# Kernel tuning notes

Measured on AMD Instinct MI355X. Metric: run time of the kernel, lower is better.

## Reference

```python
import jax, jax.numpy as jnp
import numpy as np

N = 50000      # nodes
E = 800000     # edges (avg degree 16)
F_IN = 128     # mod2_dim
DIMS = [(F_IN, 64), (64, 128), (128, 256), (256, 256)]
OUT_DIM = 1    # final_prediction: Linear(256, 1)


def setup_inputs() -> dict:
    key = jax.random.key(0)
    ks = jax.random.split(key, 16)
    inp = {
        "x": jax.random.normal(ks[0], (N, F_IN), jnp.float32),
        "edge_index": jax.random.randint(ks[1], (2, E), 0, N, dtype=jnp.int64),
        "edge_attr": jax.random.uniform(ks[2], (E,), jnp.float32),
    }
    for i, (fin, fout) in enumerate(DIMS):
        inp[f"W{i+1}"] = jax.random.normal(ks[3 + i], (fin, fout), jnp.float32) / np.sqrt(fin)
        inp[f"b{i+1}"] = jnp.zeros((fout,), jnp.float32)
    inp["Wf"] = jax.random.normal(ks[8], (256, OUT_DIM), jnp.float32) / np.sqrt(256.0)
    inp["bf"] = jnp.zeros((OUT_DIM,), jnp.float32)
    return inp


def _gcn_conv(x, src, dst, w, W, b):
    """PyG GCNConv: D^-1/2 (A + I) D^-1/2 X W + b with edge weights.
    src/dst/w already include self-loops (weight 1)."""
    h = x @ W                                            # [N, Fout]
    deg = jax.ops.segment_sum(w, dst, num_segments=N)    # weighted in-degree
    dinv = jnp.where(deg > 0, jax.lax.rsqrt(deg), 0.0)
    norm = dinv[src] * w * dinv[dst]                     # [E+N]
    msg = h[src] * norm[:, None]                         # gather + scale
    out = jax.ops.segment_sum(msg, dst, num_segments=N)  # scatter-add
    return out + b


def reference(x, edge_index, edge_attr, W1, b1, W2, b2, W3, b3, W4, b4, Wf, bf):
    loops = jnp.arange(N, dtype=edge_index.dtype)
    src = jnp.concatenate([edge_index[0], loops])
    dst = jnp.concatenate([edge_index[1], loops])
    w = jnp.concatenate([edge_attr, jnp.ones((N,), edge_attr.dtype)])

    h = x
    for W, b in ((W1, b1), (W2, b2), (W3, b3), (W4, b4)):
        h = jax.nn.relu(_gcn_conv(h, src, dst, w, W, b))
        # F.dropout with training=False -> identity (eval mode)
    out = h @ Wf + bf
    return out
```

## Files before the change

kernel.cpp:

```cpp
#include <hip/hip_runtime.h>
#include <math.h>


typedef _Float16 half8 __attribute__((ext_vector_type(8)));
typedef _Float16 half4_t __attribute__((ext_vector_type(4)));
typedef float f32x4 __attribute__((ext_vector_type(4)));

#define SCAN_CHUNK 2048
#define DEG_SCALE 67108864.0f
#define DEG_MASK ((1ULL << 42) - 1)

__global__ __launch_bounds__(256) void k_init(unsigned long long* __restrict__ packed,
                                              int n) {
    int i = blockIdx.x * 256 + threadIdx.x;
    if (i < n) packed[i] = (1ULL << 26);
}

__global__ __launch_bounds__(256) void k_count_slot(const int* __restrict__ dst,
                                                    const float* __restrict__ w,
                                                    unsigned long long* __restrict__ packed,
                                                    int* __restrict__ slot, int e) {
    int i = blockIdx.x * 256 + threadIdx.x;
    if (i < e) {
        unsigned long long wf = (unsigned long long)(w[i] * DEG_SCALE + 0.5f);
        unsigned long long old = atomicAdd(&packed[dst[i]], (1ULL << 42) | wf);
        slot[i] = (int)(old >> 42);
    }
}

__global__ __launch_bounds__(256) void k_dinv(const unsigned long long* __restrict__ packed,
                                              float* __restrict__ dinv,
                                              int* __restrict__ cnt, int n) {
    int i = blockIdx.x * 256 + threadIdx.x;
    if (i < n) {
        unsigned long long p = packed[i];
        float d = (float)((double)(p & DEG_MASK) * (1.0 / 67108864.0));
        dinv[i] = d > 0.0f ? rsqrtf(d) : 0.0f;
        cnt[i] = (int)(p >> 42);
    }
}

__global__ __launch_bounds__(256) void k_cvtw(const float* __restrict__ W1,
                                              const float* __restrict__ W2,
                                              const float* __restrict__ W3,
                                              const float* __restrict__ W4,
                                              _Float16* __restrict__ out) {
    int i = blockIdx.x * 256 + threadIdx.x;
    if (i >= 114688) return;
    const float* src; int off;
    if (i < 8192)       { src = W1; off = 0; }
    else if (i < 16384) { src = W2; off = 8192; }
    else if (i < 49152) { src = W3; off = 16384; }
    else                { src = W4; off = 49152; }
    out[i] = (_Float16)src[i - off];
}

__global__ __launch_bounds__(256) void k_scan_part(const int* __restrict__ cnt,
                                                   int* __restrict__ row_ptr,
                                                   int* __restrict__ blocksum, int n) {
    __shared__ int sp[256];
    int tid = threadIdx.x;
    int base = blockIdx.x * SCAN_CHUNK + tid * 8;
    int4 v0 = make_int4(0, 0, 0, 0), v1 = make_int4(0, 0, 0, 0);
    if (base < n) {
        v0 = *(const int4*)(cnt + base);
        v1 = *(const int4*)(cnt + base + 4);
    }
    int s = v0.x + v0.y + v0.z + v0.w + v1.x + v1.y + v1.z + v1.w;
    sp[tid] = s;
    __syncthreads();
    for (int d = 1; d < 256; d <<= 1) {
        int t = (tid >= d) ? sp[tid - d] : 0;
        __syncthreads();
        sp[tid] += t;
        __syncthreads();
    }
    int off = (tid == 0) ? 0 : sp[tid - 1];
    if (base < n) {
        int o[8] = {v0.x, v0.y, v0.z, v0.w, v1.x, v1.y, v1.z, v1.w};
        int run = off;
#pragma unroll
        for (int i = 0; i < 8; ++i) { int c = o[i]; o[i] = run; run += c; }
        *(int4*)(row_ptr + base)     = make_int4(o[0], o[1], o[2], o[3]);
        *(int4*)(row_ptr + base + 4) = make_int4(o[4], o[5], o[6], o[7]);
    }
    if (tid == 255) blocksum[blockIdx.x] = sp[255];
}

__global__ __launch_bounds__(64) void k_scan_mid(const int* __restrict__ blocksum,
                                                 int* __restrict__ blockoff, int nb) {
    int lane = threadIdx.x;
    int c = (lane < nb) ? blocksum[lane] : 0;
    int v = c;
    for (int d = 1; d < 64; d <<= 1) {
        int t = __shfl_up(v, d);
        if (lane >= d) v += t;
    }
    if (lane < nb) blockoff[lane] = v - c;
}

__global__ __launch_bounds__(256) void k_scan_add(int* __restrict__ row_ptr,
                                                  const int* __restrict__ blockoff,
                                                  int n, int total) {
    int tid = threadIdx.x;
    int base = blockIdx.x * SCAN_CHUNK + tid * 8;
    if (base < n) {
        int off = blockoff[blockIdx.x];
        int4 a = *(const int4*)(row_ptr + base);
        int4 b = *(const int4*)(row_ptr + base + 4);
        a.x += off; a.y += off; a.z += off; a.w += off;
        b.x += off; b.y += off; b.z += off; b.w += off;
        *(int4*)(row_ptr + base)     = a;
        *(int4*)(row_ptr + base + 4) = b;
    }
    if (blockIdx.x == 0 && tid == 0) row_ptr[n] = total;
}

__global__ __launch_bounds__(256) void k_fill(const int* __restrict__ src,
                                              const int* __restrict__ dst,
                                              const float* __restrict__ w,
                                              const float* __restrict__ dinv,
                                              const int* __restrict__ row_ptr,
                                              const int* __restrict__ slot,
                                              float2* __restrict__ csr, int e) {
    int i = blockIdx.x * 256 + threadIdx.x;
    if (i < e) {
        int d = dst[i], s = src[i];
        float nv = dinv[s] * w[i] * dinv[d];
        csr[row_ptr[d] + slot[i]] = make_float2(__int_as_float(s), nv);
    }
}

template <bool RELU, typename TA, bool XCD4>
__global__ __launch_bounds__(256) void gemm_mfma(const TA* __restrict__ A,
                                                 const _Float16* __restrict__ B,
                                                 const float* __restrict__ bias,
                                                 _Float16* __restrict__ C,
                                                 int M, int K, int N) {
    constexpr int PK = 72;
    __shared__ _Float16 Asl[128 * PK];
    __shared__ _Float16 Bsl[64 * PK];

    int tid = threadIdx.x;
    int w = tid >> 6, l = tid & 63;
    int row0, col0;
    if constexpr (XCD4) {
        int bid = blockIdx.x;
        int xcd = bid & 7;
        int cb = (bid >> 3) & 3;
        int rb = xcd + 8 * (bid >> 5);
        row0 = rb * 128;
        col0 = cb * 64;
    } else {
        row0 = blockIdx.x * 128;
        col0 = blockIdx.y * 64;
    }
    int wr = w * 32;
    int lr = l & 15, lg = l >> 4;

    int srow = tid >> 1;
    int skh = (tid & 1) * 32;
    int bk = tid >> 4;
    int bn = (tid & 15) * 4;

    f32x4 acc[2][4] = {};

    for (int k0 = 0; k0 < K; k0 += 64) {
        const TA* ap = A + (size_t)(row0 + srow) * K + k0 + skh;
        bool aok = (row0 + srow) < M;
#pragma unroll
        for (int i = 0; i < 4; ++i) {
            half8 h;
            if constexpr (sizeof(TA) == 4) {
                float4 v0 = aok ? *(const float4*)((const float*)ap + i * 8 + 0)
                                : make_float4(0.f, 0.f, 0.f, 0.f);
                float4 v1 = aok ? *(const float4*)((const float*)ap + i * 8 + 4)
                                : make_float4(0.f, 0.f, 0.f, 0.f);
                h[0] = (_Float16)v0.x; h[1] = (_Float16)v0.y;
                h[2] = (_Float16)v0.z; h[3] = (_Float16)v0.w;
                h[4] = (_Float16)v1.x; h[5] = (_Float16)v1.y;
                h[6] = (_Float16)v1.z; h[7] = (_Float16)v1.w;
            } else {
                h = aok ? *(const half8*)((const _Float16*)ap + i * 8)
                        : half8{0, 0, 0, 0, 0, 0, 0, 0};
            }
            *(half8*)&Asl[srow * PK + skh + i * 8] = h;
        }
#pragma unroll
        for (int r = 0; r < 4; ++r) {
            int kk = bk + r * 16;
            half4_t wv = *(const half4_t*)(B + (size_t)(k0 + kk) * N + col0 + bn);
            Bsl[(bn + 0) * PK + kk] = wv[0];
            Bsl[(bn + 1) * PK + kk] = wv[1];
            Bsl[(bn + 2) * PK + kk] = wv[2];
            Bsl[(bn + 3) * PK + kk] = wv[3];
        }
        __syncthreads();

#pragma unroll
        for (int kr = 0; kr < 2; ++kr) {
            half8 af[2], bf[4];
#pragma unroll
            for (int m = 0; m < 2; ++m)
                af[m] = *(half8*)&Asl[(wr + m * 16 + lr) * PK + kr * 32 + lg * 8];
#pragma unroll
            for (int n = 0; n < 4; ++n)
                bf[n] = *(half8*)&Bsl[(n * 16 + lr) * PK + kr * 32 + lg * 8];
#pragma unroll
            for (int m = 0; m < 2; ++m)
#pragma unroll
                for (int n = 0; n < 4; ++n)
                    acc[m][n] = __builtin_amdgcn_mfma_f32_16x16x32_f16(
                        af[m], bf[n], acc[m][n], 0, 0, 0);
        }
        __syncthreads();
    }

#pragma unroll
    for (int m = 0; m < 2; ++m) {
#pragma unroll
        for (int r = 0; r < 4; ++r) {
            int row = row0 + wr + m * 16 + lg * 4 + r;
            if (row >= M) continue;
#pragma unroll
            for (int n = 0; n < 4; ++n) {
                int col = col0 + n * 16 + lr;
                float v = acc[m][n][r];
                if (RELU) v = fmaxf(v + bias[col], 0.f);
                C[(size_t)row * N + col] = (_Float16)v;
            }
        }
    }
}

template <int FO, bool BIASRELU>
__global__ __launch_bounds__(256) void k_gather2(const int* __restrict__ row_ptr,
                                                 const float2* __restrict__ csr,
                                                 const _Float16* __restrict__ H,
                                                 const float* __restrict__ dinv,
                                                 const float* __restrict__ b,
                                                 _Float16* __restrict__ O, int n) {
    constexpr int LPE = FO / 4;
    constexpr int GRP = 64 / LPE;
    int node = blockIdx.x * 4 + (threadIdx.x >> 6);
    int lane = threadIdx.x & 63;
    if (node >= n) return;
    int grp = lane / LPE;
    int cols = (lane % LPE) * 4;

    float ax = 0.f, ay = 0.f, az = 0.f, aw = 0.f;
    int e0 = row_ptr[node], e1 = row_ptr[node + 1];

    for (int e = e0; e < e1; e += 4 * GRP) {
        float nv[4]; half4_t hv[4];
#pragma unroll
        for (int u = 0; u < 4; ++u) {
            int er = e + u * GRP + grp;
            int eg = min(er, e1 - 1);
            float2 c = csr[eg];
            hv[u] = *(const half4_t*)(H + (size_t)__float_as_int(c.x) * FO + cols);
            nv[u] = (er < e1) ? c.y : 0.f;
        }
#pragma unroll
        for (int u = 0; u < 4; ++u) {
            ax += nv[u] * (float)hv[u][0];
            ay += nv[u] * (float)hv[u][1];
            az += nv[u] * (float)hv[u][2];
            aw += nv[u] * (float)hv[u][3];
        }
    }

#pragma unroll
    for (int off = LPE; off < 64; off <<= 1) {
        ax += __shfl_down(ax, off);
        ay += __shfl_down(ay, off);
        az += __shfl_down(az, off);
        aw += __shfl_down(aw, off);
    }

    if (lane < LPE) {
        float di = dinv[node];
        float s = di * di;
        half4_t hs = *(const half4_t*)(H + (size_t)node * FO + cols);
        ax += s * (float)hs[0];
        ay += s * (float)hs[1];
        az += s * (float)hs[2];
        aw += s * (float)hs[3];
        if (BIASRELU) {
            float4 bv = *(const float4*)(b + cols);
            ax = fmaxf(ax + bv.x, 0.f);
            ay = fmaxf(ay + bv.y, 0.f);
            az = fmaxf(az + bv.z, 0.f);
            aw = fmaxf(aw + bv.w, 0.f);
        }
        half4_t o;
        o[0] = (_Float16)ax; o[1] = (_Float16)ay;
        o[2] = (_Float16)az; o[3] = (_Float16)aw;
        *(half4_t*)(O + (size_t)node * FO + cols) = o;
    }
}

__global__ __launch_bounds__(256) void k_gather_final2(const int* __restrict__ row_ptr,
                                                       const float2* __restrict__ csr,
                                                       const _Float16* __restrict__ H,
                                                       const float* __restrict__ dinv,
                                                       const float* __restrict__ b4,
                                                       const float* __restrict__ Wf,
                                                       const float* __restrict__ bf,
                                                       float* __restrict__ out, int n) {
    int node = blockIdx.x * 4 + (threadIdx.x >> 6);
    int lane = threadIdx.x & 63;
    if (node >= n) return;
    int cols = lane * 4;

    float ax = 0.f, ay = 0.f, az = 0.f, aw = 0.f;
    int e0 = row_ptr[node], e1 = row_ptr[node + 1];

    for (int e = e0; e < e1; e += 4) {
        float nv[4]; half4_t hv[4];
#pragma unroll
        for (int u = 0; u < 4; ++u) {
            int er = e + u;
            int eg = min(er, e1 - 1);
            float2 c = csr[eg];
            hv[u] = *(const half4_t*)(H + (size_t)__float_as_int(c.x) * 256 + cols);
            nv[u] = (er < e1) ? c.y : 0.f;
        }
#pragma unroll
        for (int u = 0; u < 4; ++u) {
            ax += nv[u] * (float)hv[u][0];
            ay += nv[u] * (float)hv[u][1];
            az += nv[u] * (float)hv[u][2];
            aw += nv[u] * (float)hv[u][3];
        }
    }

    float di = dinv[node];
    float s = di * di;
    half4_t hs = *(const half4_t*)(H + (size_t)node * 256 + cols);
    float4 bv = *(const float4*)(b4 + cols);
    float4 wv = *(const float4*)(Wf + cols);
    float v = fmaxf(ax + s * (float)hs[0] + bv.x, 0.f) * wv.x
            + fmaxf(ay + s * (float)hs[1] + bv.y, 0.f) * wv.y
            + fmaxf(az + s * (float)hs[2] + bv.z, 0.f) * wv.z
            + fmaxf(aw + s * (float)hs[3] + bv.w, 0.f) * wv.w;
#pragma unroll
    for (int off = 32; off > 0; off >>= 1) v += __shfl_down(v, off);
    if (lane == 0) out[node] = v + bf[0];
}


extern "C" void kernel_launch(void* const* d_in, const int* in_sizes, int n_in,
                              void* d_out, int out_size, void* d_ws, size_t ws_size,
                              hipStream_t stream) {
    const float* x    = (const float*)d_in[0];
    const int*   eidx = (const int*)d_in[1];
    const float* eatt = (const float*)d_in[2];
    const float* W1 = (const float*)d_in[3];
    const float* b1 = (const float*)d_in[4];
    const float* W2 = (const float*)d_in[5];
    const float* b2 = (const float*)d_in[6];
    const float* W3 = (const float*)d_in[7];
    const float* b3 = (const float*)d_in[8];
    const float* W4 = (const float*)d_in[9];
    const float* b4 = (const float*)d_in[10];
    const float* Wf = (const float*)d_in[11];
    const float* bf = (const float*)d_in[12];

    const int NN = in_sizes[0] / 128;
    const int NE = in_sizes[2];
    const int* src = eidx;
    const int* dst = eidx + NE;

    const int Na = (NN + 64) & ~63;
    unsigned long long* packed = (unsigned long long*)d_ws;
    float* dinv    = (float*)(packed + Na);
    int*   row_ptr = (int*)(dinv + Na);
    int*   cnt     = row_ptr + Na;
    int*   bsum    = cnt + Na;
    int*   boff    = bsum + 64;
    _Float16* wf16 = (_Float16*)(boff + 64);
    int*   slot    = (int*)(wf16 + 114688);
    float2* csr    = (float2*)(slot + ((NE + 1) & ~1));
    _Float16* bufA = (_Float16*)(csr + NE);
    _Float16* bufB = bufA + (size_t)NN * 256;

    const _Float16* W1h = wf16;
    const _Float16* W2h = wf16 + 8192;
    const _Float16* W3h = wf16 + 16384;
    const _Float16* W4h = wf16 + 49152;

    const int nscan = (NN + SCAN_CHUNK - 1) / SCAN_CHUNK;

    k_cvtw<<<448, 256, 0, stream>>>(W1, W2, W3, W4, wf16);
    k_init<<<(NN + 255) / 256, 256, 0, stream>>>(packed, NN);
    k_count_slot<<<(NE + 255) / 256, 256, 0, stream>>>(dst, eatt, packed, slot, NE);
    k_dinv<<<(NN + 255) / 256, 256, 0, stream>>>(packed, dinv, cnt, NN);
    k_scan_part<<<nscan, 256, 0, stream>>>(cnt, row_ptr, bsum, NN);
    k_scan_mid<<<1, 64, 0, stream>>>(bsum, boff, nscan);
    k_scan_add<<<nscan, 256, 0, stream>>>(row_ptr, boff, NN, NE);
    k_fill<<<(NE + 255) / 256, 256, 0, stream>>>(src, dst, eatt, dinv, row_ptr, slot, csr, NE);

    int gw = (NN + 3) / 4;
    int gx = (NN + 127) / 128;
    int gx8 = ((gx + 7) & ~7);
    int gxcd = gx8 * 4;

    gemm_mfma<false, float, false><<<dim3(gx, 1), 256, 0, stream>>>(x, W1h, nullptr, bufB, NN, 128, 64);
    k_gather2<64, true><<<gw, 256, 0, stream>>>(row_ptr, csr, bufB, dinv, b1, bufA, NN);

    k_gather2<64, false><<<gw, 256, 0, stream>>>(row_ptr, csr, bufA, dinv, nullptr, bufB, NN);
    gemm_mfma<true, _Float16, false><<<dim3(gx, 2), 256, 0, stream>>>(bufB, W2h, b2, bufA, NN, 64, 128);

    k_gather2<128, false><<<gw, 256, 0, stream>>>(row_ptr, csr, bufA, dinv, nullptr, bufB, NN);
    gemm_mfma<true, _Float16, true><<<dim3(gxcd, 1), 256, 0, stream>>>(bufB, W3h, b3, bufA, NN, 128, 256);

    gemm_mfma<false, _Float16, true><<<dim3(gxcd, 1), 256, 0, stream>>>(bufA, W4h, nullptr, bufB, NN, 256, 256);
    k_gather_final2<<<gw, 256, 0, stream>>>(row_ptr, csr, bufB, dinv, b4, Wf, bf,
                                            (float*)d_out, NN);
}
```

Baseline: 291.8 us.

## Split wide gathers into column slices across blocks with edge-parallel lanes

```diff
diff --git a/kernel.cpp b/kernel.cpp
--- a/kernel.cpp
+++ b/kernel.cpp
@@ -300,34 +300,34 @@
     }
 }
 
-__global__ __launch_bounds__(256) void k_gather_final2(const int* __restrict__ row_ptr,
-                                                       const float2* __restrict__ csr,
-                                                       const _Float16* __restrict__ H,
-                                                       const float* __restrict__ dinv,
-                                                       const float* __restrict__ b4,
-                                                       const float* __restrict__ Wf,
-                                                       const float* __restrict__ bf,
-                                                       float* __restrict__ out, int n) {
-    int node = blockIdx.x * 4 + (threadIdx.x >> 6);
+__global__ __launch_bounds__(256) void k_g128_slice(const int* __restrict__ row_ptr,
+                                                    const float2* __restrict__ csr,
+                                                    const _Float16* __restrict__ H,
+                                                    const float* __restrict__ dinv,
+                                                    _Float16* __restrict__ O, int n) {
+    int bid = blockIdx.x;
+    int s = bid & 7;
+    int node = (bid >> 3) * 4 + (threadIdx.x >> 6);
     int lane = threadIdx.x & 63;
     if (node >= n) return;
-    int cols = lane * 4;
+    int grp = lane >> 2;
+    unsigned cols = s * 16 + (lane & 3) * 4;
 
     float ax = 0.f, ay = 0.f, az = 0.f, aw = 0.f;
     int e0 = row_ptr[node], e1 = row_ptr[node + 1];
 
-    for (int e = e0; e < e1; e += 4) {
-        float nv[4]; half4_t hv[4];
-#pragma unroll
-        for (int u = 0; u < 4; ++u) {
-            int er = e + u;
+    for (int e = e0; e < e1; e += 32) {
+        float nv[2]; half4_t hv[2];
+#pragma unroll
+        for (int u = 0; u < 2; ++u) {
+            int er = e + u * 16 + grp;
             int eg = min(er, e1 - 1);
             float2 c = csr[eg];
-            hv[u] = *(const half4_t*)(H + (size_t)__float_as_int(c.x) * 256 + cols);
+            hv[u] = *(const half4_t*)(H + (unsigned)__float_as_int(c.x) * 128 + cols);
             nv[u] = (er < e1) ? c.y : 0.f;
         }
 #pragma unroll
-        for (int u = 0; u < 4; ++u) {
+        for (int u = 0; u < 2; ++u) {
             ax += nv[u] * (float)hv[u][0];
             ay += nv[u] * (float)hv[u][1];
             az += nv[u] * (float)hv[u][2];
@@ -335,18 +335,99 @@
         }
     }
 
-    float di = dinv[node];
-    float s = di * di;
-    half4_t hs = *(const half4_t*)(H + (size_t)node * 256 + cols);
-    float4 bv = *(const float4*)(b4 + cols);
-    float4 wv = *(const float4*)(Wf + cols);
-    float v = fmaxf(ax + s * (float)hs[0] + bv.x, 0.f) * wv.x
-            + fmaxf(ay + s * (float)hs[1] + bv.y, 0.f) * wv.y
-            + fmaxf(az + s * (float)hs[2] + bv.z, 0.f) * wv.z
-            + fmaxf(aw + s * (float)hs[3] + bv.w, 0.f) * wv.w;
-#pragma unroll
-    for (int off = 32; off > 0; off >>= 1) v += __shfl_down(v, off);
-    if (lane == 0) out[node] = v + bf[0];
+#pragma unroll
+    for (int off = 4; off < 64; off <<= 1) {
+        ax += __shfl_down(ax, off);
+        ay += __shfl_down(ay, off);
+        az += __shfl_down(az, off);
+        aw += __shfl_down(aw, off);
+    }
+
+    if (lane < 4) {
+        float di = dinv[node];
+        float sc = di * di;
+        half4_t hs = *(const half4_t*)(H + (unsigned)node * 128 + cols);
+        half4_t o;
+        o[0] = (_Float16)(ax + sc * (float)hs[0]);
+        o[1] = (_Float16)(ay + sc * (float)hs[1]);
+        o[2] = (_Float16)(az + sc * (float)hs[2]);
+        o[3] = (_Float16)(aw + sc * (float)hs[3]);
+        *(half4_t*)(O + (unsigned)node * 128 + cols) = o;
+    }
+}
+
+__global__ __launch_bounds__(256) void k_gf_slice(const int* __restrict__ row_ptr,
+                                                  const float2* __restrict__ csr,
+                                                  const _Float16* __restrict__ H,
+                                                  const float* __restrict__ dinv,
+                                                  const float* __restrict__ b4,
+                                                  const float* __restrict__ Wf,
+                                                  float* __restrict__ partial, int n) {
+    int bid = blockIdx.x;
+    int s = bid & 7;
+    int node = (bid >> 3) * 4 + (threadIdx.x >> 6);
+    int lane = threadIdx.x & 63;
+    if (node >= n) return;
+    int grp = lane >> 3;
+    unsigned cols = s * 32 + (lane & 7) * 4;
+
+    float ax = 0.f, ay = 0.f, az = 0.f, aw = 0.f;
+    int e0 = row_ptr[node], e1 = row_ptr[node + 1];
+
+    for (int e = e0; e < e1; e += 16) {
+        float nv[2]; half4_t hv[2];
+#pragma unroll
+        for (int u = 0; u < 2; ++u) {
+            int er = e + u * 8 + grp;
+            int eg = min(er, e1 - 1);
+            float2 c = csr[eg];
+            hv[u] = *(const half4_t*)(H + (unsigned)__float_as_int(c.x) * 256 + cols);
+            nv[u] = (er < e1) ? c.y : 0.f;
+        }
+#pragma unroll
+        for (int u = 0; u < 2; ++u) {
+            ax += nv[u] * (float)hv[u][0];
+            ay += nv[u] * (float)hv[u][1];
+            az += nv[u] * (float)hv[u][2];
+            aw += nv[u] * (float)hv[u][3];
+        }
+    }
+
+#pragma unroll
+    for (int off = 8; off < 64; off <<= 1) {
+        ax += __shfl_down(ax, off);
+        ay += __shfl_down(ay, off);
+        az += __shfl_down(az, off);
+        aw += __shfl_down(aw, off);
+    }
+
+    float v = 0.f;
+    if (lane < 8) {
+        float di = dinv[node];
+        float sc = di * di;
+        half4_t hs = *(const half4_t*)(H + (unsigned)node * 256 + cols);
+        float4 bv = *(const float4*)(b4 + cols);
+        float4 wv = *(const float4*)(Wf + cols);
+        v = fmaxf(ax + sc * (float)hs[0] + bv.x, 0.f) * wv.x
+          + fmaxf(ay + sc * (float)hs[1] + bv.y, 0.f) * wv.y
+          + fmaxf(az + sc * (float)hs[2] + bv.z, 0.f) * wv.z
+          + fmaxf(aw + sc * (float)hs[3] + bv.w, 0.f) * wv.w;
+    }
+    v += __shfl_down(v, 4);
+    v += __shfl_down(v, 2);
+    v += __shfl_down(v, 1);
+    if (lane == 0) partial[node * 8 + s] = v;
+}
+
+__global__ __launch_bounds__(256) void k_part_reduce(const float* __restrict__ partial,
+                                                     const float* __restrict__ bf,
+                                                     float* __restrict__ out, int n) {
+    int i = blockIdx.x * 256 + threadIdx.x;
+    if (i < n) {
+        float4 a = *(const float4*)(partial + i * 8);
+        float4 b = *(const float4*)(partial + i * 8 + 4);
+        out[i] = a.x + a.y + a.z + a.w + b.x + b.y + b.z + b.w + bf[0];
+    }
 }
 
 
@@ -384,6 +465,7 @@
     float2* csr    = (float2*)(slot + ((NE + 1) & ~1));
     _Float16* bufA = (_Float16*)(csr + NE);
     _Float16* bufB = bufA + (size_t)NN * 256;
+    float* partial = (float*)(bufB + (size_t)NN * 256);
 
     const _Float16* W1h = wf16;
     const _Float16* W2h = wf16 + 8192;
@@ -402,6 +484,7 @@
     k_fill<<<(NE + 255) / 256, 256, 0, stream>>>(src, dst, eatt, dinv, row_ptr, slot, csr, NE);
 
     int gw = (NN + 3) / 4;
+    int gs = 8 * ((NN + 3) / 4);
     int gx = (NN + 127) / 128;
     int gx8 = ((gx + 7) & ~7);
     int gxcd = gx8 * 4;
@@ -412,10 +495,10 @@
     k_gather2<64, false><<<gw, 256, 0, stream>>>(row_ptr, csr, bufA, dinv, nullptr, bufB, NN);
     gemm_mfma<true, _Float16, false><<<dim3(gx, 2), 256, 0, stream>>>(bufB, W2h, b2, bufA, NN, 64, 128);
 
-    k_gather2<128, false><<<gw, 256, 0, stream>>>(row_ptr, csr, bufA, dinv, nullptr, bufB, NN);
+    k_g128_slice<<<gs, 256, 0, stream>>>(row_ptr, csr, bufA, dinv, bufB, NN);
     gemm_mfma<true, _Float16, true><<<dim3(gxcd, 1), 256, 0, stream>>>(bufB, W3h, b3, bufA, NN, 128, 256);
 
     gemm_mfma<false, _Float16, true><<<dim3(gxcd, 1), 256, 0, stream>>>(bufA, W4h, nullptr, bufB, NN, 256, 256);
-    k_gather_final2<<<gw, 256, 0, stream>>>(row_ptr, csr, bufB, dinv, b4, Wf, bf,
-                                            (float*)d_out, NN);
-}
+    k_gf_slice<<<gs, 256, 0, stream>>>(row_ptr, csr, bufB, dinv, b4, Wf, partial, NN);
+    k_part_reduce<<<(NN + 255) / 256, 256, 0, stream>>>(partial, bf, (float*)d_out, NN);
+}
```

Result: slower. 445.8 us (+52.8%).

## Store layer-4 features as 32-column panels and split final gather into slices

Applied to the files above, without the earlier changes.

```diff
diff --git a/kernel.cpp b/kernel.cpp
--- a/kernel.cpp
+++ b/kernel.cpp
@@ -131,7 +131,7 @@
     }
 }
 
-template <bool RELU, typename TA, bool XCD4>
+template <bool RELU, typename TA, bool XCD4, bool PANEL>
 __global__ __launch_bounds__(256) void gemm_mfma(const TA* __restrict__ A,
                                                  const _Float16* __restrict__ B,
                                                  const float* __restrict__ bias,
@@ -227,7 +227,12 @@
                 int col = col0 + n * 16 + lr;
                 float v = acc[m][n][r];
                 if (RELU) v = fmaxf(v + bias[col], 0.f);
-                C[(size_t)row * N + col] = (_Float16)v;
+                if constexpr (PANEL) {
+                    int s = col >> 5;
+                    C[((size_t)s * M + row) * 32 + (col & 31)] = (_Float16)v;
+                } else {
+                    C[(size_t)row * N + col] = (_Float16)v;
+                }
             }
         }
     }
@@ -300,30 +305,34 @@
     }
 }
 
-__global__ __launch_bounds__(256) void k_gather_final2(const int* __restrict__ row_ptr,
-                                                       const float2* __restrict__ csr,
-                                                       const _Float16* __restrict__ H,
-                                                       const float* __restrict__ dinv,
-                                                       const float* __restrict__ b4,
-                                                       const float* __restrict__ Wf,
-                                                       const float* __restrict__ bf,
-                                                       float* __restrict__ out, int n) {
-    int node = blockIdx.x * 4 + (threadIdx.x >> 6);
+__global__ __launch_bounds__(256) void k_gf_slice(const int* __restrict__ row_ptr,
+                                                  const float2* __restrict__ csr,
+                                                  const _Float16* __restrict__ Hp,
+                                                  const float* __restrict__ dinv,
+                                                  const float* __restrict__ b4,
+                                                  const float* __restrict__ Wf,
+                                                  float* __restrict__ partial, int n) {
+    int bid = blockIdx.x;
+    int s = bid & 7;
+    int node = (bid >> 3) * 4 + (threadIdx.x >> 6);
     int lane = threadIdx.x & 63;
     if (node >= n) return;
-    int cols = lane * 4;
+    int grp = lane >> 3;
+    unsigned coff = (lane & 7) * 4;
+    const _Float16* H = Hp + (size_t)s * n * 32;
 
     float ax = 0.f, ay = 0.f, az = 0.f, aw = 0.f;
     int e0 = row_ptr[node], e1 = row_ptr[node + 1];
 
-    for (int e = e0; e < e1; e += 4) {
+    for (int e = e0; e < e1; e += 32) {
         float nv[4]; half4_t hv[4];
 #pragma unroll
         for (int u = 0; u < 4; ++u) {
-            int er = e + u;
+            int er = e + u * 8 + grp;
             int eg = min(er, e1 - 1);
-            float2 c = csr[eg];
-            hv[u] = *(const half4_t*)(H + (size_t)__float_as_int(c.x) * 256 + cols);
+            double cd = __builtin_nontemporal_load((const double*)(csr + eg));
+            float2 c = *(float2*)&cd;
+            hv[u] = *(const half4_t*)(H + (unsigned)__float_as_int(c.x) * 32 + coff);
             nv[u] = (er < e1) ? c.y : 0.f;
         }
 #pragma unroll
@@ -335,18 +344,42 @@
         }
     }
 
-    float di = dinv[node];
-    float s = di * di;
-    half4_t hs = *(const half4_t*)(H + (size_t)node * 256 + cols);
-    float4 bv = *(const float4*)(b4 + cols);
-    float4 wv = *(const float4*)(Wf + cols);
-    float v = fmaxf(ax + s * (float)hs[0] + bv.x, 0.f) * wv.x
-            + fmaxf(ay + s * (float)hs[1] + bv.y, 0.f) * wv.y
-            + fmaxf(az + s * (float)hs[2] + bv.z, 0.f) * wv.z
-            + fmaxf(aw + s * (float)hs[3] + bv.w, 0.f) * wv.w;
-#pragma unroll
-    for (int off = 32; off > 0; off >>= 1) v += __shfl_down(v, off);
-    if (lane == 0) out[node] = v + bf[0];
+#pragma unroll
+    for (int off = 8; off < 64; off <<= 1) {
+        ax += __shfl_down(ax, off);
+        ay += __shfl_down(ay, off);
+        az += __shfl_down(az, off);
+        aw += __shfl_down(aw, off);
+    }
+
+    float v = 0.f;
+    if (lane < 8) {
+        float di = dinv[node];
+        float sc = di * di;
+        half4_t hs = *(const half4_t*)(H + (unsigned)node * 32 + coff);
+        unsigned cols = s * 32 + coff;
+        float4 bv = *(const float4*)(b4 + cols);
+        float4 wv = *(const float4*)(Wf + cols);
+        v = fmaxf(ax + sc * (float)hs[0] + bv.x, 0.f) * wv.x
+          + fmaxf(ay + sc * (float)hs[1] + bv.y, 0.f) * wv.y
+          + fmaxf(az + sc * (float)hs[2] + bv.z, 0.f) * wv.z
+          + fmaxf(aw + sc * (float)hs[3] + bv.w, 0.f) * wv.w;
+    }
+    v += __shfl_down(v, 4);
+    v += __shfl_down(v, 2);
+    v += __shfl_down(v, 1);
+    if (lane == 0) partial[node * 8 + s] = v;
+}
+
+__global__ __launch_bounds__(256) void k_part_reduce(const float* __restrict__ partial,
+                                                     const float* __restrict__ bf,
+                                                     float* __restrict__ out, int n) {
+    int i = blockIdx.x * 256 + threadIdx.x;
+    if (i < n) {
+        float4 a = *(const float4*)(partial + i * 8);
+        float4 b = *(const float4*)(partial + i * 8 + 4);
+        out[i] = a.x + a.y + a.z + a.w + b.x + b.y + b.z + b.w + bf[0];
+    }
 }
 
 
@@ -384,6 +417,7 @@
     float2* csr    = (float2*)(slot + ((NE + 1) & ~1));
     _Float16* bufA = (_Float16*)(csr + NE);
     _Float16* bufB = bufA + (size_t)NN * 256;
+    float* partial = (float*)(bufB + (size_t)NN * 256);
 
     const _Float16* W1h = wf16;
     const _Float16* W2h = wf16 + 8192;
@@ -402,20 +436,21 @@
     k_fill<<<(NE + 255) / 256, 256, 0, stream>>>(src, dst, eatt, dinv, row_ptr, slot, csr, NE);
 
     int gw = (NN + 3) / 4;
+    int gs = 8 * ((NN + 3) / 4);
     int gx = (NN + 127) / 128;
     int gx8 = ((gx + 7) & ~7);
     int gxcd = gx8 * 4;
 
-    gemm_mfma<false, float, false><<<dim3(gx, 1), 256, 0, stream>>>(x, W1h, nullptr, bufB, NN, 128, 64);
+    gemm_mfma<false, float, false, false><<<dim3(gx, 1), 256, 0, stream>>>(x, W1h, nullptr, bufB, NN, 128, 64);
     k_gather2<64, true><<<gw, 256, 0, stream>>>(row_ptr, csr, bufB, dinv, b1, bufA, NN);
 
     k_gather2<64, false><<<gw, 256, 0, stream>>>(row_ptr, csr, bufA, dinv, nullptr, bufB, NN);
-    gemm_mfma<true, _Float16, false><<<dim3(gx, 2), 256, 0, stream>>>(bufB, W2h, b2, bufA, NN, 64, 128);
+    gemm_mfma<true, _Float16, false, false><<<dim3(gx, 2), 256, 0, stream>>>(bufB, W2h, b2, bufA, NN, 64, 128);
 
     k_gather2<128, false><<<gw, 256, 0, stream>>>(row_ptr, csr, bufA, dinv, nullptr, bufB, NN);
-    gemm_mfma<true, _Float16, true><<<dim3(gxcd, 1), 256, 0, stream>>>(bufB, W3h, b3, bufA, NN, 128, 256);
-
-    gemm_mfma<false, _Float16, true><<<dim3(gxcd, 1), 256, 0, stream>>>(bufA, W4h, nullptr, bufB, NN, 256, 256);
-    k_gather_final2<<<gw, 256, 0, stream>>>(row_ptr, csr, bufB, dinv, b4, Wf, bf,
-                                            (float*)d_out, NN);
-}
+    gemm_mfma<true, _Float16, true, false><<<dim3(gxcd, 1), 256, 0, stream>>>(bufB, W3h, b3, bufA, NN, 128, 256);
+
+    gemm_mfma<false, _Float16, true, true><<<dim3(gxcd, 1), 256, 0, stream>>>(bufA, W4h, nullptr, bufB, NN, 256, 256);
+    k_gf_slice<<<gs, 256, 0, stream>>>(row_ptr, csr, bufB, dinv, b4, Wf, partial, NN);
+    k_part_reduce<<<(NN + 255) / 256, 256, 0, stream>>>(partial, bf, (float*)d_out, NN);
+}
```

New measurement: 395.3 us. 35.5% more time.

## Fuse preprocessing kernels and widen gather loads to 16-byte half8 with edge-split lanes

Applied to the files above, without the earlier changes.

```diff
diff --git a/kernel.cpp b/kernel.cpp
--- a/kernel.cpp
+++ b/kernel.cpp
@@ -9,11 +9,27 @@
 #define SCAN_CHUNK 2048
 #define DEG_SCALE 67108864.0f
 #define DEG_MASK ((1ULL << 42) - 1)
-
-__global__ __launch_bounds__(256) void k_init(unsigned long long* __restrict__ packed,
-                                              int n) {
+#define NW 114688
+
+__global__ __launch_bounds__(256) void k_cvtw_init(const float* __restrict__ W1,
+                                                   const float* __restrict__ W2,
+                                                   const float* __restrict__ W3,
+                                                   const float* __restrict__ W4,
+                                                   _Float16* __restrict__ out,
+                                                   unsigned long long* __restrict__ packed,
+                                                   int n) {
     int i = blockIdx.x * 256 + threadIdx.x;
-    if (i < n) packed[i] = (1ULL << 26);
+    if (i < NW) {
+        const float* src; int off;
+        if (i < 8192)       { src = W1; off = 0; }
+        else if (i < 16384) { src = W2; off = 8192; }
+        else if (i < 49152) { src = W3; off = 16384; }
+        else                { src = W4; off = 49152; }
+        out[i] = (_Float16)src[i - off];
+    } else {
+        int j = i - NW;
+        if (j < n) packed[j] = (1ULL << 26);
+    }
 }
 
 __global__ __launch_bounds__(256) void k_count_slot(const int* __restrict__ dst,
@@ -28,45 +44,24 @@
     }
 }
 
-__global__ __launch_bounds__(256) void k_dinv(const unsigned long long* __restrict__ packed,
-                                              float* __restrict__ dinv,
-                                              int* __restrict__ cnt, int n) {
-    int i = blockIdx.x * 256 + threadIdx.x;
-    if (i < n) {
-        unsigned long long p = packed[i];
-        float d = (float)((double)(p & DEG_MASK) * (1.0 / 67108864.0));
-        dinv[i] = d > 0.0f ? rsqrtf(d) : 0.0f;
-        cnt[i] = (int)(p >> 42);
-    }
-}
-
-__global__ __launch_bounds__(256) void k_cvtw(const float* __restrict__ W1,
-                                              const float* __restrict__ W2,
-                                              const float* __restrict__ W3,
-                                              const float* __restrict__ W4,
-                                              _Float16* __restrict__ out) {
-    int i = blockIdx.x * 256 + threadIdx.x;
-    if (i >= 114688) return;
-    const float* src; int off;
-    if (i < 8192)       { src = W1; off = 0; }
-    else if (i < 16384) { src = W2; off = 8192; }
-    else if (i < 49152) { src = W3; off = 16384; }
-    else                { src = W4; off = 49152; }
-    out[i] = (_Float16)src[i - off];
-}
-
-__global__ __launch_bounds__(256) void k_scan_part(const int* __restrict__ cnt,
+__global__ __launch_bounds__(256) void k_dinv_scan(const unsigned long long* __restrict__ packed,
+                                                   float* __restrict__ dinv,
                                                    int* __restrict__ row_ptr,
                                                    int* __restrict__ blocksum, int n) {
     __shared__ int sp[256];
     int tid = threadIdx.x;
     int base = blockIdx.x * SCAN_CHUNK + tid * 8;
-    int4 v0 = make_int4(0, 0, 0, 0), v1 = make_int4(0, 0, 0, 0);
+    int c[8] = {0, 0, 0, 0, 0, 0, 0, 0};
     if (base < n) {
-        v0 = *(const int4*)(cnt + base);
-        v1 = *(const int4*)(cnt + base + 4);
-    }
-    int s = v0.x + v0.y + v0.z + v0.w + v1.x + v1.y + v1.z + v1.w;
+#pragma unroll
+        for (int j = 0; j < 8; ++j) {
+            unsigned long long p = packed[base + j];
+            float d = (float)((double)(p & DEG_MASK) * (1.0 / 67108864.0));
+            dinv[base + j] = d > 0.0f ? rsqrtf(d) : 0.0f;
+            c[j] = (int)(p >> 42);
+        }
+    }
+    int s = c[0] + c[1] + c[2] + c[3] + c[4] + c[5] + c[6] + c[7];
     sp[tid] = s;
     __syncthreads();
     for (int d = 1; d < 256; d <<= 1) {
@@ -77,35 +72,34 @@
     }
     int off = (tid == 0) ? 0 : sp[tid - 1];
     if (base < n) {
-        int o[8] = {v0.x, v0.y, v0.z, v0.w, v1.x, v1.y, v1.z, v1.w};
+        int o[8];
         int run = off;
 #pragma unroll
-        for (int i = 0; i < 8; ++i) { int c = o[i]; o[i] = run; run += c; }
+        for (int j = 0; j < 8; ++j) { o[j] = run; run += c[j]; }
         *(int4*)(row_ptr + base)     = make_int4(o[0], o[1], o[2], o[3]);
         *(int4*)(row_ptr + base + 4) = make_int4(o[4], o[5], o[6], o[7]);
     }
     if (tid == 255) blocksum[blockIdx.x] = sp[255];
 }
 
-__global__ __launch_bounds__(64) void k_scan_mid(const int* __restrict__ blocksum,
-                                                 int* __restrict__ blockoff, int nb) {
-    int lane = threadIdx.x;
-    int c = (lane < nb) ? blocksum[lane] : 0;
-    int v = c;
-    for (int d = 1; d < 64; d <<= 1) {
-        int t = __shfl_up(v, d);
-        if (lane >= d) v += t;
-    }
-    if (lane < nb) blockoff[lane] = v - c;
-}
-
 __global__ __launch_bounds__(256) void k_scan_add(int* __restrict__ row_ptr,
-                                                  const int* __restrict__ blockoff,
-                                                  int n, int total) {
+                                                  const int* __restrict__ blocksum,
+                                                  int n, int total, int nb) {
+    __shared__ int bo[64];
     int tid = threadIdx.x;
+    if (tid < 64) {
+        int c = (tid < nb) ? blocksum[tid] : 0;
+        int v = c;
+        for (int d = 1; d < 64; d <<= 1) {
+            int t = __shfl_up(v, d);
+            if (tid >= d) v += t;
+        }
+        bo[tid] = v - c;
+    }
+    __syncthreads();
     int base = blockIdx.x * SCAN_CHUNK + tid * 8;
     if (base < n) {
-        int off = blockoff[blockIdx.x];
+        int off = bo[blockIdx.x];
         int4 a = *(const int4*)(row_ptr + base);
         int4 b = *(const int4*)(row_ptr + base + 4);
         a.x += off; a.y += off; a.z += off; a.w += off;
@@ -300,52 +294,113 @@
     }
 }
 
-__global__ __launch_bounds__(256) void k_gather_final2(const int* __restrict__ row_ptr,
-                                                       const float2* __restrict__ csr,
-                                                       const _Float16* __restrict__ H,
-                                                       const float* __restrict__ dinv,
-                                                       const float* __restrict__ b4,
-                                                       const float* __restrict__ Wf,
-                                                       const float* __restrict__ bf,
-                                                       float* __restrict__ out, int n) {
+__global__ __launch_bounds__(256) void k_g128_h8(const int* __restrict__ row_ptr,
+                                                 const float2* __restrict__ csr,
+                                                 const _Float16* __restrict__ H,
+                                                 const float* __restrict__ dinv,
+                                                 _Float16* __restrict__ O, int n) {
     int node = blockIdx.x * 4 + (threadIdx.x >> 6);
     int lane = threadIdx.x & 63;
     if (node >= n) return;
-    int cols = lane * 4;
-
-    float ax = 0.f, ay = 0.f, az = 0.f, aw = 0.f;
+    int grp = lane >> 4;
+    unsigned cols = (lane & 15) * 8;
+
+    float acc[8] = {};
     int e0 = row_ptr[node], e1 = row_ptr[node + 1];
 
-    for (int e = e0; e < e1; e += 4) {
-        float nv[4]; half4_t hv[4];
+    for (int e = e0; e < e1; e += 16) {
+        float nv[4]; half8 hv[4];
 #pragma unroll
         for (int u = 0; u < 4; ++u) {
-            int er = e + u;
+            int er = e + u * 4 + grp;
             int eg = min(er, e1 - 1);
             float2 c = csr[eg];
-            hv[u] = *(const half4_t*)(H + (size_t)__float_as_int(c.x) * 256 + cols);
+            hv[u] = *(const half8*)(H + (unsigned)__float_as_int(c.x) * 128 + cols);
             nv[u] = (er < e1) ? c.y : 0.f;
         }
 #pragma unroll
+        for (int u = 0; u < 4; ++u)
+#pragma unroll
+            for (int j = 0; j < 8; ++j)
+                acc[j] += nv[u] * (float)hv[u][j];
+    }
+
+#pragma unroll
+    for (int j = 0; j < 8; ++j) {
+        acc[j] += __shfl_down(acc[j], 16);
+        acc[j] += __shfl_down(acc[j], 32);
+    }
+
+    if (lane < 16) {
+        float di = dinv[node];
+        float sc = di * di;
+        half8 hs = *(const half8*)(H + (unsigned)node * 128 + cols);
+        half8 o;
+#pragma unroll
+        for (int j = 0; j < 8; ++j)
+            o[j] = (_Float16)(acc[j] + sc * (float)hs[j]);
+        *(half8*)(O + (unsigned)node * 128 + cols) = o;
+    }
+}
+
+__global__ __launch_bounds__(256) void k_gfinal_h8(const int* __restrict__ row_ptr,
+                                                   const float2* __restrict__ csr,
+                                                   const _Float16* __restrict__ H,
+                                                   const float* __restrict__ dinv,
+                                                   const float* __restrict__ b4,
+                                                   const float* __restrict__ Wf,
+                                                   const float* __restrict__ bf,
+                                                   float* __restrict__ out, int n) {
+    int node = blockIdx.x * 4 + (threadIdx.x >> 6);
+    int lane = threadIdx.x & 63;
+    if (node >= n) return;
+    int grp = lane >> 5;
+    unsigned cols = (lane & 31) * 8;
+
+    float acc[8] = {};
+    int e0 = row_ptr[node], e1 = row_ptr[node + 1];
+
+    for (int e = e0; e < e1; e += 8) {
+        float nv[4]; half8 hv[4];
+#pragma unroll
         for (int u = 0; u < 4; ++u) {
-            ax += nv[u] * (float)hv[u][0];
-            ay += nv[u] * (float)hv[u][1];
-            az += nv[u] * (float)hv[u][2];
-            aw += nv[u] * (float)hv[u][3];
-        }
-    }
-
-    float di = dinv[node];
-    float s = di * di;
-    half4_t hs = *(const half4_t*)(H + (size_t)node * 256 + cols);
-    float4 bv = *(const float4*)(b4 + cols);
-    float4 wv = *(const float4*)(Wf + cols);
-    float v = fmaxf(ax + s * (float)hs[0] + bv.x, 0.f) * wv.x
-            + fmaxf(ay + s * (float)hs[1] + bv.y, 0.f) * wv.y
-            + fmaxf(az + s * (float)hs[2] + bv.z, 0.f) * wv.z
-            + fmaxf(aw + s * (float)hs[3] + bv.w, 0.f) * wv.w;
-#pragma unroll
-    for (int off = 32; off > 0; off >>= 1) v += __shfl_down(v, off);
+            int er = e + u * 2 + grp;
+            int eg = min(er, e1 - 1);
+            float2 c = csr[eg];
+            hv[u] = *(const half8*)(H + (unsigned)__float_as_int(c.x) * 256 + cols);
+            nv[u] = (er < e1) ? c.y : 0.f;
+        }
+#pragma unroll
+        for (int u = 0; u < 4; ++u)
+#pragma unroll
+            for (int j = 0; j < 8; ++j)
+                acc[j] += nv[u] * (float)hv[u][j];
+    }
+
+#pragma unroll
+    for (int j = 0; j < 8; ++j)
+        acc[j] += __shfl_down(acc[j], 32);
+
+    float v = 0.f;
+    if (lane < 32) {
+        float di = dinv[node];
+        float sc = di * di;
+        half8 hs = *(const half8*)(H + (unsigned)node * 256 + cols);
+        float4 bv0 = *(const float4*)(b4 + cols);
+        float4 bv1 = *(const float4*)(b4 + cols + 4);
+        float4 wv0 = *(const float4*)(Wf + cols);
+        float4 wv1 = *(const float4*)(Wf + cols + 4);
+        float bb[8] = {bv0.x, bv0.y, bv0.z, bv0.w, bv1.x, bv1.y, bv1.z, bv1.w};
+        float ww[8] = {wv0.x, wv0.y, wv0.z, wv0.w, wv1.x, wv1.y, wv1.z, wv1.w};
+#pragma unroll
+        for (int j = 0; j < 8; ++j)
+            v += fmaxf(acc[j] + sc * (float)hs[j] + bb[j], 0.f) * ww[j];
+    }
+    v += __shfl_down(v, 16);
+    v += __shfl_down(v, 8);
+    v += __shfl_down(v, 4);
+    v += __shfl_down(v, 2);
+    v += __shfl_down(v, 1);
     if (lane == 0) out[node] = v + bf[0];
 }
 
@@ -376,11 +431,9 @@
     unsigned long long* packed = (unsigned long long*)d_ws;
     float* dinv    = (float*)(packed + Na);
     int*   row_ptr = (int*)(dinv + Na);
-    int*   cnt     = row_ptr + Na;
-    int*   bsum    = cnt + Na;
-    int*   boff    = bsum + 64;
-    _Float16* wf16 = (_Float16*)(boff + 64);
-    int*   slot    = (int*)(wf16 + 114688);
+    int*   bsum    = row_ptr + Na;
+    _Float16* wf16 = (_Float16*)(bsum + 64);
+    int*   slot    = (int*)(wf16 + NW);
     float2* csr    = (float2*)(slot + ((NE + 1) & ~1));
     _Float16* bufA = (_Float16*)(csr + NE);
     _Float16* bufB = bufA + (size_t)NN * 256;
@@ -392,13 +445,10 @@
 
     const int nscan = (NN + SCAN_CHUNK - 1) / SCAN_CHUNK;
 
-    k_cvtw<<<448, 256, 0, stream>>>(W1, W2, W3, W4, wf16);
-    k_init<<<(NN + 255) / 256, 256, 0, stream>>>(packed, NN);
+    k_cvtw_init<<<(NW + NN + 255) / 256, 256, 0, stream>>>(W1, W2, W3, W4, wf16, packed, NN);
     k_count_slot<<<(NE + 255) / 256, 256, 0, stream>>>(dst, eatt, packed, slot, NE);
-    k_dinv<<<(NN + 255) / 256, 256, 0, stream>>>(packed, dinv, cnt, NN);
-    k_scan_part<<<nscan, 256, 0, stream>>>(cnt, row_ptr, bsum, NN);
-    k_scan_mid<<<1, 64, 0, stream>>>(bsum, boff, nscan);
-    k_scan_add<<<nscan, 256, 0, stream>>>(row_ptr, boff, NN, NE);
+    k_dinv_scan<<<nscan, 256, 0, stream>>>(packed, dinv, row_ptr, bsum, NN);
+    k_scan_add<<<nscan, 256, 0, stream>>>(row_ptr, bsum, NN, NE, nscan);
     k_fill<<<(NE + 255) / 256, 256, 0, stream>>>(src, dst, eatt, dinv, row_ptr, slot, csr, NE);
 
     int gw = (NN + 3) / 4;
@@ -412,10 +462,10 @@
     k_gather2<64, false><<<gw, 256, 0, stream>>>(row_ptr, csr, bufA, dinv, nullptr, bufB, NN);
     gemm_mfma<true, _Float16, false><<<dim3(gx, 2), 256, 0, stream>>>(bufB, W2h, b2, bufA, NN, 64, 128);
 
-    k_gather2<128, false><<<gw, 256, 0, stream>>>(row_ptr, csr, bufA, dinv, nullptr, bufB, NN);
+    k_g128_h8<<<gw, 256, 0, stream>>>(row_ptr, csr, bufA, dinv, bufB, NN);
     gemm_mfma<true, _Float16, true><<<dim3(gxcd, 1), 256, 0, stream>>>(bufB, W3h, b3, bufA, NN, 128, 256);
 
     gemm_mfma<false, _Float16, true><<<dim3(gxcd, 1), 256, 0, stream>>>(bufA, W4h, nullptr, bufB, NN, 256, 256);
-    k_gather_final2<<<gw, 256, 0, stream>>>(row_ptr, csr, bufB, dinv, b4, Wf, bf,
-                                            (float*)d_out, NN);
-}
+    k_gfinal_h8<<<gw, 256, 0, stream>>>(row_ptr, csr, bufB, dinv, b4, Wf, bf,
+                                        (float*)d_out, NN);
+}
```

Measured after the change: 276.2 us. -5.3%, faster.
